# Kernel tuning notes

Hardware: AMD Instinct MI355X
Metric: run time of the kernel (lower is better)

## Reference

```python
import jax, jax.numpy as jnp
import numpy as np
import math

# module hyperparams (from init_kwargs)
H = 4          # num_heads
HID = 128      # hid_dim
DK = HID // H  # embed_time_k = 32
DIM = 64       # input_dim (value feature dim)
OUT = 128      # output_dim
NEG = -1e30


def setup_inputs() -> dict:
    key = jax.random.key(0)
    ks = jax.random.split(key, 10)
    B, SQ, SK = 16, 128, 256
    query = jax.random.normal(ks[0], (B, SQ, HID), jnp.float32)
    k_in = jax.random.normal(ks[1], (B, SK, HID), jnp.float32)
    value = jax.random.normal(ks[2], (B, SK, DIM), jnp.float32)
    mask = jax.random.randint(ks[3], (B, SK, DIM), 0, 2).astype(jnp.int32)
    s = 1.0 / math.sqrt(HID)
    Wq = jax.random.uniform(ks[4], (HID, HID), jnp.float32, -s, s)
    bq = jax.random.uniform(ks[5], (HID,), jnp.float32, -s, s)
    Wk = jax.random.uniform(ks[6], (HID, HID), jnp.float32, -s, s)
    bk = jax.random.uniform(ks[7], (HID,), jnp.float32, -s, s)
    so = 1.0 / math.sqrt(DIM * H)
    Wo = jax.random.uniform(ks[8], (OUT, DIM * H), jnp.float32, -so, so)
    bo = jax.random.uniform(ks[9], (OUT,), jnp.float32, -so, so)
    return {"query": query, "key": k_in, "value": value, "mask": mask,
            "Wq": Wq, "bq": bq, "Wk": Wk, "bk": bk, "Wo": Wo, "bo": bo}


def reference(query, key, value, mask, Wq, bq, Wk, bk, Wo, bo):
    B, SQ, _ = query.shape
    _, SK, D = value.shape
    # project and split heads: (B, S, HID) -> (B, H, S, DK)
    q = (query @ Wq.T + bq).reshape(B, SQ, H, DK).transpose(0, 2, 1, 3)
    k = (key @ Wk.T + bk).reshape(B, SK, H, DK).transpose(0, 2, 1, 3)
    # scores: (B, H, SQ, SK)
    scores = jnp.einsum('bhqd,bhkd->bhqk', q, k) / math.sqrt(DK)
    # per-channel mask: scores expand to (B, H, SQ, SK, D)
    m = (mask[:, None, None, :, :] != 0)  # (B,1,1,SK,D)
    scores5 = jnp.where(m, scores[..., None], NEG)
    # softmax over seq_k axis (axis=-2)
    p = jax.nn.softmax(scores5, axis=-2)
    # weighted sum over seq_k: (B, H, SQ, D)
    x = jnp.sum(p * value[:, None, None, :, :], axis=-2)
    # merge heads: (B, SQ, H*D) then output projection
    x = x.transpose(0, 2, 1, 3).reshape(B, SQ, H * D)
    return x @ Wo.T + bo
```

## Files before the change

kernel.cpp:

```cpp
#include <hip/hip_runtime.h>
#include <hip/hip_bf16.h>
#include <math.h>

#define B    16
#define SEQK 256
#define HID  128
#define NH   4
#define DK   32
#define DIM  64
#define OUTD 128

typedef __attribute__((ext_vector_type(8))) short short8;
typedef __attribute__((ext_vector_type(4))) float floatx4;

#define NB_PROJ 384
#define NB_MVT  64
#define NB_WOB  32
#define NB_SETUP (NB_PROJ + NB_MVT + NB_WOB)

__device__ __forceinline__ unsigned f2bf(float x) {
    union { float f; unsigned u; } v; v.f = x;
    return (v.u + 0x7FFFu + ((v.u >> 16) & 1u)) >> 16;
}

__global__ __launch_bounds__(256) void setup_kernel(
    const float* __restrict__ query, const float* __restrict__ key,
    const float* __restrict__ value, const int* __restrict__ mask,
    const float* __restrict__ Wq, const float* __restrict__ bq,
    const float* __restrict__ Wk, const float* __restrict__ bk,
    const float* __restrict__ Wo,
    float* __restrict__ qp, float* __restrict__ kp_t,
    unsigned* __restrict__ mvt_u, unsigned* __restrict__ wob_u)
{
    __shared__ float smem[16 * 128 + 32 * 130];
    const int bid = blockIdx.x;
    const int t   = threadIdx.x;

    if (bid < NB_PROJ) {
        float* in16 = smem;
        float* Wt   = smem + 2048;
        const int r0 = bid * 16;
        const bool isQ = (r0 < 2048);
        const float4* src4 = (const float4*)(isQ ? (query + r0 * 128)
                                                 : (key + (r0 - 2048) * 128));
        {
            float4* in4 = (float4*)in16;
            in4[t]       = src4[t];
            in4[t + 256] = src4[t + 256];
        }
        const float* Wsrc = isQ ? Wq : Wk;
        const int j  = t & 127;
        const int rg = (t >> 7) * 8;
        const float bias = isQ ? bq[j] : bk[j];
        float acc[8];
#pragma unroll
        for (int r = 0; r < 8; ++r) acc[r] = bias;

        for (int ic = 0; ic < 4; ++ic) {
            __syncthreads();
            {
                const int i4 = t & 7, jg = t >> 3;
#pragma unroll
                for (int jj = 0; jj < 4; ++jj) {
                    const int jw = jg + jj * 32;
                    const float4 w = *(const float4*)(Wsrc + jw * 128 + ic * 32 + i4 * 4);
                    Wt[(i4 * 4 + 0) * 130 + jw] = w.x;
                    Wt[(i4 * 4 + 1) * 130 + jw] = w.y;
                    Wt[(i4 * 4 + 2) * 130 + jw] = w.z;
                    Wt[(i4 * 4 + 3) * 130 + jw] = w.w;
                }
            }
            __syncthreads();
#pragma unroll 2
            for (int i4 = 0; i4 < 8; ++i4) {
                const float w0 = Wt[(i4 * 4 + 0) * 130 + j];
                const float w1 = Wt[(i4 * 4 + 1) * 130 + j];
                const float w2 = Wt[(i4 * 4 + 2) * 130 + j];
                const float w3 = Wt[(i4 * 4 + 3) * 130 + j];
#pragma unroll
                for (int r = 0; r < 8; ++r) {
                    const float4 xv = ((const float4*)(in16 + (rg + r) * 128))[ic * 8 + i4];
                    acc[r] = fmaf(xv.x, w0, fmaf(xv.y, w1, fmaf(xv.z, w2, fmaf(xv.w, w3, acc[r]))));
                }
            }
        }

        if (isQ) {
            const float scale = 0.17677669529663687f;
#pragma unroll
            for (int r = 0; r < 8; ++r) qp[(r0 + rg + r) * 128 + j] = acc[r] * scale;
        } else {
#pragma unroll
            for (int r = 0; r < 8; ++r) {
                const int row = r0 - 2048 + rg + r;
                const int bb = row >> 8, k = row & 255;
                kp_t[(bb * 128 + j) * 256 + k] = acc[r];
            }
        }
    } else if (bid < NB_PROJ + NB_MVT) {
        const int bb = (bid - NB_PROJ) >> 2, kt = (bid - NB_PROJ) & 3;
        const int c4 = t & 15, kp2 = t >> 4;
#pragma unroll
        for (int rr = 0; rr < 2; ++rr) {
            const int kpair = kp2 + rr * 16;
            const int k0 = kt * 64 + kpair * 2;
            const float4 v0 = *(const float4*)(value + (bb * 256 + k0) * 64 + c4 * 4);
            const float4 v1 = *(const float4*)(value + (bb * 256 + k0 + 1) * 64 + c4 * 4);
            const int4   m0 = *(const int4*)(mask + (bb * 256 + k0) * 64 + c4 * 4);
            const int4   m1 = *(const int4*)(mask + (bb * 256 + k0 + 1) * 64 + c4 * 4);
            const float a0[4] = {v0.x, v0.y, v0.z, v0.w};
            const float a1[4] = {v1.x, v1.y, v1.z, v1.w};
            const int   i0[4] = {m0.x, m0.y, m0.z, m0.w};
            const int   i1[4] = {m1.x, m1.y, m1.z, m1.w};
#pragma unroll
            for (int cc = 0; cc < 4; ++cc) {
                const int c = c4 * 4 + cc;
                const unsigned mv = (f2bf(i1[cc] ? a1[cc] : 0.f) << 16)
                                  |  f2bf(i0[cc] ? a0[cc] : 0.f);
                const unsigned ff = ((i1[cc] ? 0x3F80u : 0u) << 16)
                                  |  (i0[cc] ? 0x3F80u : 0u);
                mvt_u[(bb * 128 + c) * 128 + kt * 32 + kpair]      = mv;
                mvt_u[(bb * 128 + 64 + c) * 128 + kt * 32 + kpair] = ff;
            }
        }
    } else {
        const int idx4 = (bid - NB_PROJ - NB_MVT) * 256 + t;
        const float4 w = ((const float4*)Wo)[idx4];
        uint2 p;
        p.x = (f2bf(w.y) << 16) | f2bf(w.x);
        p.y = (f2bf(w.w) << 16) | f2bf(w.z);
        ((uint2*)wob_u)[idx4] = p;
    }
}

__global__ __launch_bounds__(256) void attn_kernel(
    const float* __restrict__ qp, const float* __restrict__ kp_t,
    const short* __restrict__ mvt_s, const short* __restrict__ wob_s,
    const float* __restrict__ bo, float* __restrict__ out)
{
    const int qt = blockIdx.x, b = blockIdx.y;
    const int q0 = qt * 8;
    const int t = threadIdx.x, h = t >> 6, L = t & 63;

    __shared__ float qs[NH * 32 * 12];
    __shared__ short es[NH * 16 * 264];
    __shared__ short xs[16 * 264];

    {
        const int j = t & 127, qg = t >> 7;
        const int hh = j >> 5, ii = j & 31;
#pragma unroll
        for (int e = 0; e < 4; ++e) {
            const int q = qg * 4 + e;
            qs[hh * 384 + ii * 12 + q] = qp[(b * 128 + q0 + q) * 128 + j];
        }
    }
    __syncthreads();

    float s[8][4];
#pragma unroll
    for (int q = 0; q < 8; ++q)
#pragma unroll
        for (int kk = 0; kk < 4; ++kk) s[q][kk] = 0.f;
    {
        const float* kpb = kp_t + (b * 128 + h * 32) * 256 + L * 4;
        const float* qb  = qs + h * 384;
#pragma unroll 4
        for (int i = 0; i < 32; ++i) {
            const float4 kv = *(const float4*)(kpb + i * 256);
            const float4 qa = *(const float4*)(qb + i * 12);
            const float4 qc = *(const float4*)(qb + i * 12 + 4);
            const float qv[8] = {qa.x, qa.y, qa.z, qa.w, qc.x, qc.y, qc.z, qc.w};
            const float kw[4] = {kv.x, kv.y, kv.z, kv.w};
#pragma unroll
            for (int q = 0; q < 8; ++q)
#pragma unroll
                for (int kk = 0; kk < 4; ++kk)
                    s[q][kk] = fmaf(qv[q], kw[kk], s[q][kk]);
        }
    }

#pragma unroll
    for (int q = 0; q < 8; ++q) {
        float m = fmaxf(fmaxf(s[q][0], s[q][1]), fmaxf(s[q][2], s[q][3]));
#pragma unroll
        for (int off = 32; off > 0; off >>= 1) m = fmaxf(m, __shfl_xor(m, off, 64));
        const unsigned e01 = (f2bf(__expf(s[q][1] - m)) << 16) | f2bf(__expf(s[q][0] - m));
        const unsigned e23 = (f2bf(__expf(s[q][3] - m)) << 16) | f2bf(__expf(s[q][2] - m));
        *(uint2*)&es[h * 4224 + q * 264 + L * 4] = make_uint2(e01, e23);
    }

    const int lq = L & 15, lk = (L >> 4) * 8;
    floatx4 pv[8];
#pragma unroll
    for (int tt = 0; tt < 8; ++tt) pv[tt] = (floatx4){0.f, 0.f, 0.f, 0.f};
    {
        const short* eb = es + h * 4224 + lq * 264;
        const short* mb = mvt_s + (b * 128) * 256 + lk;
#pragma unroll
        for (int c8 = 0; c8 < 8; ++c8) {
            const short8 a = *(const short8*)(eb + c8 * 32 + lk);
#pragma unroll
            for (int tt = 0; tt < 8; ++tt) {
                const short8 bf = *(const short8*)(mb + (tt * 16 + lq) * 256 + c8 * 32);
                pv[tt] = __builtin_amdgcn_mfma_f32_16x16x32_bf16(a, bf, pv[tt], 0, 0, 0);
            }
        }
    }
    if ((L >> 4) < 2) {
#pragma unroll
        for (int tt = 0; tt < 4; ++tt)
#pragma unroll
            for (int r = 0; r < 4; ++r) {
                const int row = (L >> 4) * 4 + r;
                xs[row * 264 + h * 64 + tt * 16 + lq] =
                    (short)f2bf(pv[tt][r] / pv[tt + 4][r]);
            }
    }
    __syncthreads();

    floatx4 oa[2];
    oa[0] = (floatx4){0.f, 0.f, 0.f, 0.f};
    oa[1] = (floatx4){0.f, 0.f, 0.f, 0.f};
    {
        const short* xb = xs + lq * 264;
#pragma unroll
        for (int j8 = 0; j8 < 8; ++j8) {
            const short8 a = *(const short8*)(xb + j8 * 32 + lk);
#pragma unroll
            for (int w = 0; w < 2; ++w) {
                const int o = (h * 2 + w) * 16 + lq;
                const short8 bf = *(const short8*)(wob_s + o * 256 + j8 * 32 + lk);
                oa[w] = __builtin_amdgcn_mfma_f32_16x16x32_bf16(a, bf, oa[w], 0, 0, 0);
            }
        }
    }
    if ((L >> 4) < 2) {
#pragma unroll
        for (int w = 0; w < 2; ++w) {
            const int o = (h * 2 + w) * 16 + lq;
            const float bov = bo[o];
#pragma unroll
            for (int r = 0; r < 4; ++r) {
                const int row = (L >> 4) * 4 + r;
                out[(b * 128 + q0 + row) * 128 + o] = oa[w][r] + bov;
            }
        }
    }
}

extern "C" void kernel_launch(void* const* d_in, const int* in_sizes, int n_in,
                              void* d_out, int out_size, void* d_ws, size_t ws_size,
                              hipStream_t stream)
{
    const float* query = (const float*)d_in[0];
    const float* key   = (const float*)d_in[1];
    const float* value = (const float*)d_in[2];
    const int*   mask  = (const int*)d_in[3];
    const float* Wq    = (const float*)d_in[4];
    const float* bq    = (const float*)d_in[5];
    const float* Wk    = (const float*)d_in[6];
    const float* bk    = (const float*)d_in[7];
    const float* Wo    = (const float*)d_in[8];
    const float* bo    = (const float*)d_in[9];
    float* out = (float*)d_out;

    float* ws        = (float*)d_ws;
    float* qp        = ws;
    float* kp_t      = qp + 262144;
    unsigned* mvt_u  = (unsigned*)(kp_t + 524288);
    unsigned* wob_u  = mvt_u + 262144;

    setup_kernel<<<NB_SETUP, 256, 0, stream>>>(query, key, value, mask,
                                               Wq, bq, Wk, bk, Wo,
                                               qp, kp_t, mvt_u, wob_u);
    attn_kernel<<<dim3(16, B), 256, 0, stream>>>(qp, kp_t,
                                                 (const short*)mvt_u,
                                                 (const short*)wob_u, bo, out);
}
```

Baseline: 103.7 us.

## Fuse setup and attention kernels into one cooperative launch with grid sync

Merges the projection/packing kernel and the attention kernel into one kernel that is launched cooperatively, with a grid-wide barrier between the phases. If the cooperative launch fails it falls back to two ordinary launches selected by a phase argument. The goal is to remove the second kernel launch and the gap between the two kernels. In exchange it pays for a grid sync across 480 blocks, and occupancy is constrained by a launch bound of two blocks per CU plus about 48KB of shared memory.

```diff
diff --git a/kernel.cpp b/kernel.cpp
--- a/kernel.cpp
+++ b/kernel.cpp
@@ -1,6 +1,9 @@
 #include <hip/hip_runtime.h>
 #include <hip/hip_bf16.h>
+#include <hip/hip_cooperative_groups.h>
 #include <math.h>
+
+namespace cg = cooperative_groups;
 
 #define B    16
 #define SEQK 256
@@ -17,134 +20,143 @@
 #define NB_MVT  64
 #define NB_WOB  32
 #define NB_SETUP (NB_PROJ + NB_MVT + NB_WOB)
+#define NB_ATTN 256
 
 __device__ __forceinline__ unsigned f2bf(float x) {
     union { float f; unsigned u; } v; v.f = x;
     return (v.u + 0x7FFFu + ((v.u >> 16) & 1u)) >> 16;
 }
 
-__global__ __launch_bounds__(256) void setup_kernel(
+__global__ __launch_bounds__(256, 2) void fused_kernel(
     const float* __restrict__ query, const float* __restrict__ key,
     const float* __restrict__ value, const int* __restrict__ mask,
     const float* __restrict__ Wq, const float* __restrict__ bq,
     const float* __restrict__ Wk, const float* __restrict__ bk,
-    const float* __restrict__ Wo,
+    const float* __restrict__ Wo, const float* __restrict__ bo,
     float* __restrict__ qp, float* __restrict__ kp_t,
-    unsigned* __restrict__ mvt_u, unsigned* __restrict__ wob_u)
+    unsigned* __restrict__ mvt_u, unsigned* __restrict__ wob_u,
+    float* __restrict__ out, int phase)
 {
-    __shared__ float smem[16 * 128 + 32 * 130];
+    __shared__ __align__(16) char smem_raw[48384];
     const int bid = blockIdx.x;
     const int t   = threadIdx.x;
 
-    if (bid < NB_PROJ) {
-        float* in16 = smem;
-        float* Wt   = smem + 2048;
-        const int r0 = bid * 16;
-        const bool isQ = (r0 < 2048);
-        const float4* src4 = (const float4*)(isQ ? (query + r0 * 128)
-                                                 : (key + (r0 - 2048) * 128));
-        {
-            float4* in4 = (float4*)in16;
-            in4[t]       = src4[t];
-            in4[t + 256] = src4[t + 256];
-        }
-        const float* Wsrc = isQ ? Wq : Wk;
-        const int j  = t & 127;
-        const int rg = (t >> 7) * 8;
-        const float bias = isQ ? bq[j] : bk[j];
-        float acc[8];
-#pragma unroll
-        for (int r = 0; r < 8; ++r) acc[r] = bias;
-
-        for (int ic = 0; ic < 4; ++ic) {
-            __syncthreads();
+    if (phase != 2) {
+        if (bid < NB_PROJ) {
+            float* in16 = (float*)smem_raw;
+            float* Wt   = in16 + 2048;
+            const int r0 = bid * 16;
+            const bool isQ = (r0 < 2048);
+            const float4* src4 = (const float4*)(isQ ? (query + r0 * 128)
+                                                     : (key + (r0 - 2048) * 128));
             {
-                const int i4 = t & 7, jg = t >> 3;
-#pragma unroll
-                for (int jj = 0; jj < 4; ++jj) {
-                    const int jw = jg + jj * 32;
-                    const float4 w = *(const float4*)(Wsrc + jw * 128 + ic * 32 + i4 * 4);
-                    Wt[(i4 * 4 + 0) * 130 + jw] = w.x;
-                    Wt[(i4 * 4 + 1) * 130 + jw] = w.y;
-                    Wt[(i4 * 4 + 2) * 130 + jw] = w.z;
-                    Wt[(i4 * 4 + 3) * 130 + jw] = w.w;
+                float4* in4 = (float4*)in16;
+                in4[t]       = src4[t];
+                in4[t + 256] = src4[t + 256];
+            }
+            const float* Wsrc = isQ ? Wq : Wk;
+            const int j  = t & 127;
+            const int rg = (t >> 7) * 8;
+            const float bias = isQ ? bq[j] : bk[j];
+            float acc[8];
+#pragma unroll
+            for (int r = 0; r < 8; ++r) acc[r] = bias;
+
+            for (int ic = 0; ic < 4; ++ic) {
+                __syncthreads();
+                {
+                    const int i4 = t & 7, jg = t >> 3;
+#pragma unroll
+                    for (int jj = 0; jj < 4; ++jj) {
+                        const int jw = jg + jj * 32;
+                        const float4 w = *(const float4*)(Wsrc + jw * 128 + ic * 32 + i4 * 4);
+                        Wt[(i4 * 4 + 0) * 130 + jw] = w.x;
+                        Wt[(i4 * 4 + 1) * 130 + jw] = w.y;
+                        Wt[(i4 * 4 + 2) * 130 + jw] = w.z;
+                        Wt[(i4 * 4 + 3) * 130 + jw] = w.w;
+                    }
                 }
-            }
-            __syncthreads();
+                __syncthreads();
 #pragma unroll 2
-            for (int i4 = 0; i4 < 8; ++i4) {
-                const float w0 = Wt[(i4 * 4 + 0) * 130 + j];
-                const float w1 = Wt[(i4 * 4 + 1) * 130 + j];
-                const float w2 = Wt[(i4 * 4 + 2) * 130 + j];
-                const float w3 = Wt[(i4 * 4 + 3) * 130 + j];
+                for (int i4 = 0; i4 < 8; ++i4) {
+                    const float w0 = Wt[(i4 * 4 + 0) * 130 + j];
+                    const float w1 = Wt[(i4 * 4 + 1) * 130 + j];
+                    const float w2 = Wt[(i4 * 4 + 2) * 130 + j];
+                    const float w3 = Wt[(i4 * 4 + 3) * 130 + j];
+#pragma unroll
+                    for (int r = 0; r < 8; ++r) {
+                        const float4 xv = ((const float4*)(in16 + (rg + r) * 128))[ic * 8 + i4];
+                        acc[r] = fmaf(xv.x, w0, fmaf(xv.y, w1, fmaf(xv.z, w2, fmaf(xv.w, w3, acc[r]))));
+                    }
+                }
+            }
+
+            if (isQ) {
+                const float scale = 0.17677669529663687f;
+#pragma unroll
+                for (int r = 0; r < 8; ++r) qp[(r0 + rg + r) * 128 + j] = acc[r] * scale;
+            } else {
 #pragma unroll
                 for (int r = 0; r < 8; ++r) {
-                    const float4 xv = ((const float4*)(in16 + (rg + r) * 128))[ic * 8 + i4];
-                    acc[r] = fmaf(xv.x, w0, fmaf(xv.y, w1, fmaf(xv.z, w2, fmaf(xv.w, w3, acc[r]))));
+                    const int row = r0 - 2048 + rg + r;
+                    const int bb = row >> 8, k = row & 255;
+                    kp_t[(bb * 128 + j) * 256 + k] = acc[r];
                 }
             }
-        }
-
-        if (isQ) {
-            const float scale = 0.17677669529663687f;
-#pragma unroll
-            for (int r = 0; r < 8; ++r) qp[(r0 + rg + r) * 128 + j] = acc[r] * scale;
+        } else if (bid < NB_PROJ + NB_MVT) {
+            const int bb = (bid - NB_PROJ) >> 2, kt = (bid - NB_PROJ) & 3;
+            const int c4 = t & 15, kp2 = t >> 4;
+#pragma unroll
+            for (int rr = 0; rr < 2; ++rr) {
+                const int kpair = kp2 + rr * 16;
+                const int k0 = kt * 64 + kpair * 2;
+                const float4 v0 = *(const float4*)(value + (bb * 256 + k0) * 64 + c4 * 4);
+                const float4 v1 = *(const float4*)(value + (bb * 256 + k0 + 1) * 64 + c4 * 4);
+                const int4   m0 = *(const int4*)(mask + (bb * 256 + k0) * 64 + c4 * 4);
+                const int4   m1 = *(const int4*)(mask + (bb * 256 + k0 + 1) * 64 + c4 * 4);
+                const float a0[4] = {v0.x, v0.y, v0.z, v0.w};
+                const float a1[4] = {v1.x, v1.y, v1.z, v1.w};
+                const int   i0[4] = {m0.x, m0.y, m0.z, m0.w};
+                const int   i1[4] = {m1.x, m1.y, m1.z, m1.w};
+#pragma unroll
+                for (int cc = 0; cc < 4; ++cc) {
+                    const int c = c4 * 4 + cc;
+                    const unsigned mv = (f2bf(i1[cc] ? a1[cc] : 0.f) << 16)
+                                      |  f2bf(i0[cc] ? a0[cc] : 0.f);
+                    const unsigned ff = ((i1[cc] ? 0x3F80u : 0u) << 16)
+                                      |  (i0[cc] ? 0x3F80u : 0u);
+                    mvt_u[(bb * 128 + c) * 128 + kt * 32 + kpair]      = mv;
+                    mvt_u[(bb * 128 + 64 + c) * 128 + kt * 32 + kpair] = ff;
+                }
+            }
         } else {
-#pragma unroll
-            for (int r = 0; r < 8; ++r) {
-                const int row = r0 - 2048 + rg + r;
-                const int bb = row >> 8, k = row & 255;
-                kp_t[(bb * 128 + j) * 256 + k] = acc[r];
-            }
-        }
-    } else if (bid < NB_PROJ + NB_MVT) {
-        const int bb = (bid - NB_PROJ) >> 2, kt = (bid - NB_PROJ) & 3;
-        const int c4 = t & 15, kp2 = t >> 4;
-#pragma unroll
-        for (int rr = 0; rr < 2; ++rr) {
-            const int kpair = kp2 + rr * 16;
-            const int k0 = kt * 64 + kpair * 2;
-            const float4 v0 = *(const float4*)(value + (bb * 256 + k0) * 64 + c4 * 4);
-            const float4 v1 = *(const float4*)(value + (bb * 256 + k0 + 1) * 64 + c4 * 4);
-            const int4   m0 = *(const int4*)(mask + (bb * 256 + k0) * 64 + c4 * 4);
-            const int4   m1 = *(const int4*)(mask + (bb * 256 + k0 + 1) * 64 + c4 * 4);
-            const float a0[4] = {v0.x, v0.y, v0.z, v0.w};
-            const float a1[4] = {v1.x, v1.y, v1.z, v1.w};
-            const int   i0[4] = {m0.x, m0.y, m0.z, m0.w};
-            const int   i1[4] = {m1.x, m1.y, m1.z, m1.w};
-#pragma unroll
-            for (int cc = 0; cc < 4; ++cc) {
-                const int c = c4 * 4 + cc;
-                const unsigned mv = (f2bf(i1[cc] ? a1[cc] : 0.f) << 16)
-                                  |  f2bf(i0[cc] ? a0[cc] : 0.f);
-                const unsigned ff = ((i1[cc] ? 0x3F80u : 0u) << 16)
-                                  |  (i0[cc] ? 0x3F80u : 0u);
-                mvt_u[(bb * 128 + c) * 128 + kt * 32 + kpair]      = mv;
-                mvt_u[(bb * 128 + 64 + c) * 128 + kt * 32 + kpair] = ff;
-            }
-        }
-    } else {
-        const int idx4 = (bid - NB_PROJ - NB_MVT) * 256 + t;
-        const float4 w = ((const float4*)Wo)[idx4];
-        uint2 p;
-        p.x = (f2bf(w.y) << 16) | f2bf(w.x);
-        p.y = (f2bf(w.w) << 16) | f2bf(w.z);
-        ((uint2*)wob_u)[idx4] = p;
-    }
-}
-
-__global__ __launch_bounds__(256) void attn_kernel(
-    const float* __restrict__ qp, const float* __restrict__ kp_t,
-    const short* __restrict__ mvt_s, const short* __restrict__ wob_s,
-    const float* __restrict__ bo, float* __restrict__ out)
-{
-    const int qt = blockIdx.x, b = blockIdx.y;
+            const int idx4 = (bid - NB_PROJ - NB_MVT) * 256 + t;
+            const float4 w = ((const float4*)Wo)[idx4];
+            uint2 p;
+            p.x = (f2bf(w.y) << 16) | f2bf(w.x);
+            p.y = (f2bf(w.w) << 16) | f2bf(w.z);
+            ((uint2*)wob_u)[idx4] = p;
+        }
+    }
+
+    if (phase == 0) {
+        __threadfence();
+        cg::this_grid().sync();
+    }
+    if (phase == 1) return;
+    if (bid >= NB_ATTN) return;
+
+    const short* mvt_s = (const short*)mvt_u;
+    const short* wob_s = (const short*)wob_u;
+    const int b  = bid & 15, qt = bid >> 4;
     const int q0 = qt * 8;
-    const int t = threadIdx.x, h = t >> 6, L = t & 63;
-
-    __shared__ float qs[NH * 32 * 12];
-    __shared__ short es[NH * 16 * 264];
-    __shared__ short xs[16 * 264];
+    const int h  = t >> 6, L = t & 63;
+
+    float* qs = (float*)smem_raw;
+    short* es = (short*)(smem_raw + 6144);
+    short* xs = (short*)(smem_raw + 6144 + 33792);
+
+    if (phase == 0) __syncthreads();
 
     {
         const int j = t & 127, qg = t >> 7;
@@ -265,16 +277,28 @@
     const float* bo    = (const float*)d_in[9];
     float* out = (float*)d_out;
 
-    float* ws        = (float*)d_ws;
-    float* qp        = ws;
-    float* kp_t      = qp + 262144;
-    unsigned* mvt_u  = (unsigned*)(kp_t + 524288);
-    unsigned* wob_u  = mvt_u + 262144;
-
-    setup_kernel<<<NB_SETUP, 256, 0, stream>>>(query, key, value, mask,
-                                               Wq, bq, Wk, bk, Wo,
-                                               qp, kp_t, mvt_u, wob_u);
-    attn_kernel<<<dim3(16, B), 256, 0, stream>>>(qp, kp_t,
-                                                 (const short*)mvt_u,
-                                                 (const short*)wob_u, bo, out);
+    float* ws       = (float*)d_ws;
+    float* qp       = ws;
+    float* kp_t     = qp + 262144;
+    unsigned* mvt_u = (unsigned*)(kp_t + 524288);
+    unsigned* wob_u = mvt_u + 262144;
+
+    int phase0 = 0;
+    void* args[] = {
+        (void*)&query, (void*)&key, (void*)&value, (void*)&mask,
+        (void*)&Wq, (void*)&bq, (void*)&Wk, (void*)&bk, (void*)&Wo, (void*)&bo,
+        (void*)&qp, (void*)&kp_t, (void*)&mvt_u, (void*)&wob_u, (void*)&out,
+        (void*)&phase0
+    };
+    hipError_t err = hipLaunchCooperativeKernel((const void*)fused_kernel,
+                                                dim3(NB_SETUP), dim3(256),
+                                                args, 0, stream);
+    if (err != hipSuccess) {
+        fused_kernel<<<NB_SETUP, 256, 0, stream>>>(query, key, value, mask,
+                                                   Wq, bq, Wk, bk, Wo, bo,
+                                                   qp, kp_t, mvt_u, wob_u, out, 1);
+        fused_kernel<<<NB_ATTN, 256, 0, stream>>>(query, key, value, mask,
+                                                  Wq, bq, Wk, bk, Wo, bo,
+                                                  qp, kp_t, mvt_u, wob_u, out, 2);
+    }
 }
```

Result: slower. 231.7 us (+123.4%).
